# Performance work log

Hardware: AMD Instinct MI355X
Metric: run time of the kernel (lower is better)

Reference implementation:

```python
import jax, jax.numpy as jnp
import numpy as np

N = 10000        # nodes
E = 320000       # edges (avg degree 32)
W = 256          # width (assert width >= 256)
H = 8            # num_head (RESCALE_EDGE assumed (1,1) -> nhead=8, dhead=32)
D = W // H       # per-head dim
BOND = 33        # EMBED_BOND[0]
BAG = 3          # indices per edge bag
EPS_GN = 1e-5


def setup_inputs() -> dict:
    key = jax.random.key(0)
    ks = jax.random.split(key, 12)
    x = jax.random.normal(ks[0], (N, W), dtype=jnp.float32)
    edge_idx = jax.random.randint(ks[1], (2, E), 0, N)
    edge_attr = jax.random.randint(ks[2], (E, BAG), 0, BOND)
    # node in-degree wrt scatter target edge_idx[1], clamped to >= 1
    deg = jax.ops.segment_sum(jnp.ones((E,), jnp.float32), edge_idx[1], num_segments=N)
    deg = jnp.maximum(deg, 1.0)
    s = 1.0 / np.sqrt(W)
    W_src = jax.random.normal(ks[3], (W, W), dtype=jnp.float32) * s
    W_tgt = jax.random.normal(ks[4], (W, W), dtype=jnp.float32) * s
    emb = jax.random.normal(ks[5], (BOND, W), dtype=jnp.float32) * 0.02
    emb = emb.at[0].set(0.0)  # padding_idx=0 row is zeros
    sd = 1.0 / np.sqrt(D)
    W_gate = jax.random.normal(ks[6], (H, D, D), dtype=jnp.float32) * sd  # grouped conv1d k=1
    W_val = jax.random.normal(ks[7], (H, D, D), dtype=jnp.float32) * sd
    W_post = jax.random.normal(ks[8], (W, W), dtype=jnp.float32) * s
    deg_param = jnp.zeros((W,), jnp.float32) - 0.01  # DegreeLayer degree_init
    return {"x": x, "deg": deg, "edge_idx": edge_idx, "edge_attr": edge_attr,
            "W_src": W_src, "W_tgt": W_tgt, "emb": emb,
            "W_gate": W_gate, "W_val": W_val, "W_post": W_post,
            "deg_param": deg_param}


def reference(x, deg, edge_idx, edge_attr, W_src, W_tgt, emb, W_gate, W_val, W_post, deg_param):
    # src/tgt 1x1 Conv1d == per-node linear, then edge gather
    xs = x @ W_src.T                      # [N, W]
    xt = x @ W_tgt.T                      # [N, W]
    xx = xs[edge_idx[0]] + xt[edge_idx[1]]  # [E, W]

    # EmbeddingBag(mode='mean', padding_idx=0): padded entries excluded
    mask = (edge_attr != 0).astype(xx.dtype)            # [E, BAG]
    bag = jnp.einsum('ebc,eb->ec', emb[edge_attr], mask)  # [E, W]
    cnt = jnp.maximum(mask.sum(-1, keepdims=True), 1.0)
    gate_bias = bag / cnt

    # GroupNorm(H, W, affine=False) over [E, W, 1]
    xg = xx.reshape(-1, H, D)
    mu = xg.mean(-1, keepdims=True)
    var = xg.var(-1, keepdims=True)
    xn = (xg - mu) / jnp.sqrt(var + EPS_GN)              # [E, H, D]

    # gated grouped 1x1 convs (dropout is identity at eval)
    gin = xn + gate_bias.reshape(-1, H, D)
    gate = jax.nn.relu(jnp.einsum('ehd,hfd->ehf', gin, W_gate))
    val = jnp.einsum('ehd,hfd->ehf', xn, W_val)
    act = (gate * val).reshape(-1, W)                    # [E, W]
    out_e = act @ W_post.T                               # [E, W]

    # scatter-sum to nodes, then degree rescale
    agg = jax.ops.segment_sum(out_e, edge_idx[1], num_segments=x.shape[0])
    return jnp.power(deg[:, None], deg_param) * agg      # [N, W]
```

## Files before the change

kernel.cpp:

```cpp
#include <hip/hip_runtime.h>

#define WID 256
#define EPS_GN 1e-5f

typedef __bf16 v8bf __attribute__((ext_vector_type(8)));
typedef float  v4f  __attribute__((ext_vector_type(4)));

__device__ inline unsigned short f2b(float f) {
    unsigned int u = __builtin_bit_cast(unsigned int, f);
    unsigned int r = (u + 0x7fffu + ((u >> 16) & 1u)) >> 16;
    return (unsigned short)r;
}
__device__ inline float b2f(unsigned short s) {
    unsigned int u = (unsigned int)s << 16;
    return __builtin_bit_cast(float, u);
}
__device__ inline float lo16(unsigned int u) { return __builtin_bit_cast(float, u << 16); }
__device__ inline float hi16(unsigned int u) { return __builtin_bit_cast(float, u & 0xffff0000u); }

__global__ void prep_k(const float* __restrict__ Wsrc, const float* __restrict__ Wtgt,
                       const float* __restrict__ Wp, const float* __restrict__ Wg,
                       const float* __restrict__ Wv, const float* __restrict__ emb,
                       const int* __restrict__ eidx,
                       unsigned short* __restrict__ Wsb, unsigned short* __restrict__ Wtb,
                       unsigned short* __restrict__ Wpb, unsigned short* __restrict__ Wgb,
                       unsigned short* __restrict__ Wvb, unsigned short* __restrict__ embWgT,
                       int* __restrict__ cnt, int E, int BOND) {
    int b = blockIdx.x, t = threadIdx.x;
    if (b < 256) {
        int i = b * 256 + t;
        Wsb[i] = f2b(Wsrc[i]); Wtb[i] = f2b(Wtgt[i]); Wpb[i] = f2b(Wp[i]);
        if (i < 8192) { Wgb[i] = f2b(Wg[i]); Wvb[i] = f2b(Wv[i]); }
    } else {
        int k = b - 256;
        float s = 0.f;
        if (k < BOND) {
            int h = t >> 5, f = t & 31;
            const float* er = emb + (size_t)k * WID + h * 32;
            const float* wr = Wg + h * 1024 + f * 32;
#pragma unroll
            for (int d = 0; d < 32; d++) s += er[d] * wr[d];
        }
        embWgT[t * 64 + k] = f2b(s);
    }
    for (int i = b * 256 + t; i < E; i += 320 * 256)
        atomicAdd(&cnt[eidx[E + i]], 1);
}

__global__ void scan_k(const int* __restrict__ cnt, int* __restrict__ cur, int N) {
    __shared__ int part[1024];
    int t = threadIdx.x;
    int C = (N + 1023) / 1024;
    int s = 0;
    for (int i = 0; i < C; i++) { int idx = t * C + i; if (idx < N) s += cnt[idx]; }
    part[t] = s;
    __syncthreads();
    for (int d = 1; d < 1024; d <<= 1) {
        int v = (t >= d) ? part[t - d] : 0;
        __syncthreads();
        part[t] += v;
        __syncthreads();
    }
    int base = (t == 0) ? 0 : part[t - 1];
    for (int i = 0; i < C; i++) {
        int idx = t * C + i;
        if (idx < N) { cur[idx] = base; base += cnt[idx]; }
    }
}

__global__ void scat_k(const int* __restrict__ eidx, int* __restrict__ cur,
                       int* __restrict__ perm, int E) {
    int i = blockIdx.x * 256 + threadIdx.x;
    if (i < E) { int p = atomicAdd(&cur[eidx[E + i]], 1); perm[p] = i; }
}

__global__ __launch_bounds__(256, 2)
void proj_k(const float* __restrict__ x, const unsigned short* __restrict__ Wsb,
            const unsigned short* __restrict__ Wtb, unsigned short* __restrict__ xsb,
            unsigned short* __restrict__ xtb, int N) {
    __shared__ unsigned short ab[32 * 264];
    int t = threadIdx.x;
    int n0 = blockIdx.x * 32;
#pragma unroll
    for (int ch = 0; ch < 8; ch++) {
        int flat = ch * 1024 + t * 4;
        int row = flat >> 8, col = flat & 255;
        int n = n0 + row;
        float4 v = (n < N) ? *(const float4*)&x[(size_t)n * WID + col]
                           : make_float4(0.f, 0.f, 0.f, 0.f);
        unsigned int p0 = (unsigned int)f2b(v.x) | ((unsigned int)f2b(v.y) << 16);
        unsigned int p1 = (unsigned int)f2b(v.z) | ((unsigned int)f2b(v.w) << 16);
        *(uint2*)&ab[row * 264 + col] = make_uint2(p0, p1);
    }
    __syncthreads();
    const unsigned short* Wb = blockIdx.y ? Wtb : Wsb;
    unsigned short* outp = blockIdx.y ? xtb : xsb;
    int w = t >> 6, lane = t & 63, m = lane & 15, kg = lane >> 4;
    v4f acc[2][4];
#pragma unroll
    for (int mt = 0; mt < 2; mt++)
#pragma unroll
        for (int nt = 0; nt < 4; nt++) acc[mt][nt] = (v4f){0.f, 0.f, 0.f, 0.f};
#pragma unroll
    for (int kt = 0; kt < 8; kt++) {
        int k0 = kt * 32 + kg * 8;
        v8bf a0 = *(const v8bf*)&ab[m * 264 + k0];
        v8bf a1 = *(const v8bf*)&ab[(16 + m) * 264 + k0];
#pragma unroll
        for (int nt = 0; nt < 4; nt++) {
            int j = w * 64 + nt * 16 + m;
            v8bf b = *(const v8bf*)&Wb[j * 256 + k0];
            acc[0][nt] = __builtin_amdgcn_mfma_f32_16x16x32_bf16(a0, b, acc[0][nt], 0, 0, 0);
            acc[1][nt] = __builtin_amdgcn_mfma_f32_16x16x32_bf16(a1, b, acc[1][nt], 0, 0, 0);
        }
    }
#pragma unroll
    for (int mt = 0; mt < 2; mt++)
#pragma unroll
        for (int r = 0; r < 4; r++) {
            int n = n0 + mt * 16 + kg * 4 + r;
            if (n < N)
#pragma unroll
                for (int nt = 0; nt < 4; nt++)
                    outp[(size_t)n * WID + w * 64 + nt * 16 + m] = f2b(acc[mt][nt][r]);
        }
}

__global__ __launch_bounds__(256, 6)
void edge_k(const unsigned short* __restrict__ xsb, const unsigned short* __restrict__ xtb,
            const int* __restrict__ eidx, const int* __restrict__ eattr,
            const int* __restrict__ perm, const unsigned short* __restrict__ Wgb,
            const unsigned short* __restrict__ Wvb, const unsigned short* __restrict__ embWgT,
            float* __restrict__ aggact, int E) {
    __shared__ unsigned short xxb[32 * 264];
    __shared__ unsigned short Mld[32 * 72];
    __shared__ int src_s[32], tgt_s[32];

    int t = threadIdx.x;
    int e0 = blockIdx.x * 32;
    int ne = min(32, E - e0);

    if (t < 32) {
        int p = (t < ne) ? perm[e0 + t] : -1;
        src_s[t] = (p >= 0) ? eidx[p] : 0;
        tgt_s[t] = (p >= 0) ? eidx[E + p] : 0;
        int a0 = 0, a1 = 0, a2 = 0;
        if (p >= 0) {
            const int* ap = eattr + (size_t)p * 3;
            a0 = ap[0]; a1 = ap[1]; a2 = ap[2];
        }
        unsigned int* Mr = (unsigned int*)&Mld[t * 72];
#pragma unroll
        for (int q = 0; q < 32; q++) Mr[q] = 0;
        int c = (a0 != 0) + (a1 != 0) + (a2 != 0);
        float inv = (p >= 0 && c > 0) ? 1.f / (float)c : 0.f;
        float wa = inv * (float)(1 + (a1 == a0) + (a2 == a0));
        float wb = inv * (float)(1 + (a2 == a1));
        Mld[t * 72 + a0] = f2b(wa);
        if (a1 != a0) Mld[t * 72 + a1] = f2b(wb);
        if (a2 != a0 && a2 != a1) Mld[t * 72 + a2] = f2b(inv);
    }
    __syncthreads();

    {
        int e = t >> 3, c = t & 7;
        int s = src_s[e], g = tgt_s[e];
        bool live = (e < ne);
        const uint4* ps = (const uint4*)(xsb + (size_t)s * WID);
        const uint4* pt = (const uint4*)(xtb + (size_t)g * WID);
        uint4 us[4], ut[4];
#pragma unroll
        for (int i = 0; i < 4; i++) { us[i] = ps[c + 8 * i]; ut[i] = pt[c + 8 * i]; }
        float v[4][8], sum[4], sq[4];
#pragma unroll
        for (int i = 0; i < 4; i++) {
            const unsigned int* au = (const unsigned int*)&us[i];
            const unsigned int* bu = (const unsigned int*)&ut[i];
            sum[i] = 0.f; sq[i] = 0.f;
#pragma unroll
            for (int q = 0; q < 4; q++) {
                float x0 = lo16(au[q]) + lo16(bu[q]);
                float x1 = hi16(au[q]) + hi16(bu[q]);
                if (!live) { x0 = 0.f; x1 = 0.f; }
                v[i][2 * q] = x0; v[i][2 * q + 1] = x1;
                sum[i] += x0 + x1;
                sq[i] += x0 * x0 + x1 * x1;
            }
        }
#pragma unroll
        for (int mask = 1; mask <= 2; mask <<= 1)
#pragma unroll
            for (int i = 0; i < 4; i++) {
                sum[i] += __shfl_xor(sum[i], mask);
                sq[i]  += __shfl_xor(sq[i], mask);
            }
#pragma unroll
        for (int i = 0; i < 4; i++) {
            float mu = sum[i] * (1.f / 32.f);
            float var = sq[i] * (1.f / 32.f) - mu * mu;
            float rs = rsqrtf(var + EPS_GN);
            unsigned int pk[4];
#pragma unroll
            for (int q = 0; q < 4; q++) {
                unsigned int l = f2b((v[i][2 * q] - mu) * rs);
                unsigned int h = f2b((v[i][2 * q + 1] - mu) * rs);
                pk[q] = l | (h << 16);
            }
            *(uint4*)&xxb[e * 264 + (c + 8 * i) * 8] = make_uint4(pk[0], pk[1], pk[2], pk[3]);
        }
    }
    __syncthreads();

    {
        int w = t >> 6, lane = t & 63, m = lane & 15, kg = lane >> 4;
        v8bf axn[2][2], aM[2][2];
#pragma unroll
        for (int mt = 0; mt < 2; mt++) {
            int row = mt * 16 + m;
            axn[0][mt] = *(const v8bf*)&xxb[row * 264 + (w * 2 + 0) * 32 + kg * 8];
            axn[1][mt] = *(const v8bf*)&xxb[row * 264 + (w * 2 + 1) * 32 + kg * 8];
            aM[mt][0] = *(const v8bf*)&Mld[row * 72 + kg * 8];
            aM[mt][1] = *(const v8bf*)&Mld[row * 72 + 32 + kg * 8];
        }
        v4f z = {0.f, 0.f, 0.f, 0.f};
#pragma unroll
        for (int hh = 0; hh < 2; hh++) {
            int h = w * 2 + hh;
#pragma unroll
            for (int nt = 0; nt < 2; nt++) {
                int fj = nt * 16 + m;
                int j = h * 32 + fj;
                v8bf bWg = *(const v8bf*)&Wgb[h * 1024 + fj * 32 + kg * 8];
                v8bf bWv = *(const v8bf*)&Wvb[h * 1024 + fj * 32 + kg * 8];
                v8bf bE0 = *(const v8bf*)&embWgT[j * 64 + kg * 8];
                v8bf bE1 = *(const v8bf*)&embWgT[j * 64 + 32 + kg * 8];
#pragma unroll
                for (int mt = 0; mt < 2; mt++) {
                    v4f cg = __builtin_amdgcn_mfma_f32_16x16x32_bf16(axn[hh][mt], bWg, z, 0, 0, 0);
                    cg = __builtin_amdgcn_mfma_f32_16x16x32_bf16(aM[mt][0], bE0, cg, 0, 0, 0);
                    cg = __builtin_amdgcn_mfma_f32_16x16x32_bf16(aM[mt][1], bE1, cg, 0, 0, 0);
                    v4f cv = __builtin_amdgcn_mfma_f32_16x16x32_bf16(axn[hh][mt], bWv, z, 0, 0, 0);
#pragma unroll
                    for (int r = 0; r < 4; r++) {
                        int e = mt * 16 + kg * 4 + r;
                        xxb[e * 264 + j] = f2b(fmaxf(cg[r], 0.f) * cv[r]);
                    }
                }
            }
        }
    }
    __syncthreads();

    {
        float sum = 0.f;
        int prev = __builtin_amdgcn_readfirstlane(tgt_s[0]);
        for (int e = 0; e < ne; e++) {
            int tg = __builtin_amdgcn_readfirstlane(tgt_s[e]);
            if (tg != prev) {
                atomicAdd(&aggact[(size_t)prev * WID + t], sum);
                sum = 0.f;
                prev = tg;
            }
            sum += b2f(xxb[e * 264 + t]);
        }
        atomicAdd(&aggact[(size_t)prev * WID + t], sum);
    }
}

__global__ __launch_bounds__(256, 2)
void post_k(const float* __restrict__ aggact, const unsigned short* __restrict__ Wpb,
            const float* __restrict__ deg, const float* __restrict__ dp,
            float* __restrict__ out, int N) {
    __shared__ unsigned short ab[32 * 264];
    __shared__ float degl[32];
    int t = threadIdx.x;
    int n0 = blockIdx.x * 32;
#pragma unroll
    for (int ch = 0; ch < 8; ch++) {
        int flat = ch * 1024 + t * 4;
        int row = flat >> 8, col = flat & 255;
        int n = n0 + row;
        float4 v = (n < N) ? *(const float4*)&aggact[(size_t)n * WID + col]
                           : make_float4(0.f, 0.f, 0.f, 0.f);
        unsigned int p0 = (unsigned int)f2b(v.x) | ((unsigned int)f2b(v.y) << 16);
        unsigned int p1 = (unsigned int)f2b(v.z) | ((unsigned int)f2b(v.w) << 16);
        *(uint2*)&ab[row * 264 + col] = make_uint2(p0, p1);
    }
    if (t < 32) {
        int n = n0 + t;
        degl[t] = (n < N) ? log2f(deg[n]) : 0.f;
    }
    __syncthreads();
    int w = t >> 6, lane = t & 63, m = lane & 15, kg = lane >> 4;
    v4f acc[2][4];
#pragma unroll
    for (int mt = 0; mt < 2; mt++)
#pragma unroll
        for (int nt = 0; nt < 4; nt++) acc[mt][nt] = (v4f){0.f, 0.f, 0.f, 0.f};
#pragma unroll
    for (int kt = 0; kt < 8; kt++) {
        int k0 = kt * 32 + kg * 8;
        v8bf a0 = *(const v8bf*)&ab[m * 264 + k0];
        v8bf a1 = *(const v8bf*)&ab[(16 + m) * 264 + k0];
#pragma unroll
        for (int nt = 0; nt < 4; nt++) {
            int j = w * 64 + nt * 16 + m;
            v8bf b = *(const v8bf*)&Wpb[j * 256 + k0];
            acc[0][nt] = __builtin_amdgcn_mfma_f32_16x16x32_bf16(a0, b, acc[0][nt], 0, 0, 0);
            acc[1][nt] = __builtin_amdgcn_mfma_f32_16x16x32_bf16(a1, b, acc[1][nt], 0, 0, 0);
        }
    }
    float dpv[4];
#pragma unroll
    for (int nt = 0; nt < 4; nt++) dpv[nt] = dp[w * 64 + nt * 16 + m];
#pragma unroll
    for (int mt = 0; mt < 2; mt++)
#pragma unroll
        for (int r = 0; r < 4; r++) {
            int row = mt * 16 + kg * 4 + r;
            int n = n0 + row;
            if (n < N) {
                float ld = degl[row];
#pragma unroll
                for (int nt = 0; nt < 4; nt++)
                    out[(size_t)n * WID + w * 64 + nt * 16 + m] =
                        exp2f(dpv[nt] * ld) * acc[mt][nt][r];
            }
        }
}

extern "C" void kernel_launch(void* const* d_in, const int* in_sizes, int n_in,
                              void* d_out, int out_size, void* d_ws, size_t ws_size,
                              hipStream_t stream) {
    const float* x    = (const float*)d_in[0];
    const float* deg  = (const float*)d_in[1];
    const int*   eidx = (const int*)d_in[2];
    const int*   eatt = (const int*)d_in[3];
    const float* Wsrc = (const float*)d_in[4];
    const float* Wtgt = (const float*)d_in[5];
    const float* emb  = (const float*)d_in[6];
    const float* Wg   = (const float*)d_in[7];
    const float* Wv   = (const float*)d_in[8];
    const float* Wp   = (const float*)d_in[9];
    const float* dp   = (const float*)d_in[10];
    int N = in_sizes[0] / WID;
    int E = in_sizes[2] / 2;
    int BOND = in_sizes[6] / WID;

    float* ws     = (float*)d_ws;
    float* aggact = ws;
    int*   cnt    = (int*)(aggact + (size_t)N * WID);
    int*   cur    = cnt + N;
    int*   perm   = cur + N;
    unsigned short* xsb = (unsigned short*)(perm + E);
    unsigned short* xtb = xsb + (size_t)N * WID;
    unsigned short* Wsb = xtb + (size_t)N * WID;
    unsigned short* Wtb = Wsb + 65536;
    unsigned short* Wpb = Wtb + 65536;
    unsigned short* Wgb = Wpb + 65536;
    unsigned short* Wvb = Wgb + 8192;
    unsigned short* embWgT = Wvb + 8192;

    hipMemsetAsync(aggact, 0, ((size_t)N * WID + N) * sizeof(float), stream);
    prep_k<<<320, 256, 0, stream>>>(Wsrc, Wtgt, Wp, Wg, Wv, emb, eidx,
                                    Wsb, Wtb, Wpb, Wgb, Wvb, embWgT, cnt, E, BOND);
    scan_k<<<1, 1024, 0, stream>>>(cnt, cur, N);
    scat_k<<<(E + 255) / 256, 256, 0, stream>>>(eidx, cur, perm, E);
    proj_k<<<dim3((N + 31) / 32, 2), 256, 0, stream>>>(x, Wsb, Wtb, xsb, xtb, N);
    edge_k<<<(E + 31) / 32, 256, 0, stream>>>(xsb, xtb, eidx, eatt, perm, Wgb, Wvb, embWgT, aggact, E);
    post_k<<<(N + 31) / 32, 256, 0, stream>>>(aggact, Wpb, deg, dp, (float*)d_out, N);
}
```

Baseline: 244.0 us.

## Fuse all stages into one cooperative persistent kernel with grid syncs

Replaces the memset plus six separate launches (prep, scan, scatter, proj, edge, post) with one cooperative mega-kernel. Its stages are separated by grid.sync, and the grid is sized from the occupancy query and capped at 1536 blocks. The aim is to remove launch gaps and per-kernel tail effects. The cost is grid-wide barriers, a scan done by a single block while the others wait, and reduced occupancy and parallelism in the edge phase, which now processes contiguous tile chunks per block under a lower launch bound. The old multi-kernel path stays as a fallback if the cooperative launch fails.

```diff
diff --git a/kernel.cpp b/kernel.cpp
--- a/kernel.cpp
+++ b/kernel.cpp
@@ -1,4 +1,7 @@
 #include <hip/hip_runtime.h>
+#include <hip/hip_cooperative_groups.h>
+
+namespace cg = cooperative_groups;
 
 #define WID 256
 #define EPS_GN 1e-5f
@@ -17,6 +20,359 @@
 }
 __device__ inline float lo16(unsigned int u) { return __builtin_bit_cast(float, u << 16); }
 __device__ inline float hi16(unsigned int u) { return __builtin_bit_cast(float, u & 0xffff0000u); }
+
+struct ProjSM { unsigned short ab[32 * 264]; };
+struct EdgeSM {
+    unsigned short xxb[32 * 264];
+    unsigned short Mld[32 * 72];
+    int src_s[32], tgt_s[32];
+};
+struct PostSM { unsigned short ab[32 * 264]; float degl[32]; };
+struct ScanSM { int part[256]; };
+union MegaSM { ProjSM proj; EdgeSM edge; PostSM post; ScanSM scan; };
+
+
+__device__ __forceinline__ void proj_tile(const float* __restrict__ x,
+                                          const unsigned short* __restrict__ Wb,
+                                          unsigned short* __restrict__ outp,
+                                          int N, int n0, int t, ProjSM* s) {
+#pragma unroll
+    for (int ch = 0; ch < 8; ch++) {
+        int flat = ch * 1024 + t * 4;
+        int row = flat >> 8, col = flat & 255;
+        int n = n0 + row;
+        float4 v = (n < N) ? *(const float4*)&x[(size_t)n * WID + col]
+                           : make_float4(0.f, 0.f, 0.f, 0.f);
+        unsigned int p0 = (unsigned int)f2b(v.x) | ((unsigned int)f2b(v.y) << 16);
+        unsigned int p1 = (unsigned int)f2b(v.z) | ((unsigned int)f2b(v.w) << 16);
+        *(uint2*)&s->ab[row * 264 + col] = make_uint2(p0, p1);
+    }
+    __syncthreads();
+    int w = t >> 6, lane = t & 63, m = lane & 15, kg = lane >> 4;
+    v4f acc[2][4];
+#pragma unroll
+    for (int mt = 0; mt < 2; mt++)
+#pragma unroll
+        for (int nt = 0; nt < 4; nt++) acc[mt][nt] = (v4f){0.f, 0.f, 0.f, 0.f};
+#pragma unroll
+    for (int kt = 0; kt < 8; kt++) {
+        int k0 = kt * 32 + kg * 8;
+        v8bf a0 = *(const v8bf*)&s->ab[m * 264 + k0];
+        v8bf a1 = *(const v8bf*)&s->ab[(16 + m) * 264 + k0];
+#pragma unroll
+        for (int nt = 0; nt < 4; nt++) {
+            int j = w * 64 + nt * 16 + m;
+            v8bf b = *(const v8bf*)&Wb[j * 256 + k0];
+            acc[0][nt] = __builtin_amdgcn_mfma_f32_16x16x32_bf16(a0, b, acc[0][nt], 0, 0, 0);
+            acc[1][nt] = __builtin_amdgcn_mfma_f32_16x16x32_bf16(a1, b, acc[1][nt], 0, 0, 0);
+        }
+    }
+#pragma unroll
+    for (int mt = 0; mt < 2; mt++)
+#pragma unroll
+        for (int r = 0; r < 4; r++) {
+            int n = n0 + mt * 16 + kg * 4 + r;
+            if (n < N)
+#pragma unroll
+                for (int nt = 0; nt < 4; nt++)
+                    outp[(size_t)n * WID + w * 64 + nt * 16 + m] = f2b(acc[mt][nt][r]);
+        }
+    __syncthreads();
+}
+
+__device__ __forceinline__ void edge_tile(const unsigned short* __restrict__ xsb,
+                                          const unsigned short* __restrict__ xtb,
+                                          const int* __restrict__ eidx,
+                                          const int* __restrict__ eattr,
+                                          const int* __restrict__ perm,
+                                          const unsigned short* __restrict__ Wgb,
+                                          const unsigned short* __restrict__ Wvb,
+                                          const unsigned short* __restrict__ embWgT,
+                                          float* __restrict__ aggact,
+                                          int E, int e0, int t, EdgeSM* s) {
+    int ne = min(32, E - e0);
+
+    if (t < 32) {
+        int p = (t < ne) ? perm[e0 + t] : -1;
+        s->src_s[t] = (p >= 0) ? eidx[p] : 0;
+        s->tgt_s[t] = (p >= 0) ? eidx[E + p] : 0;
+        int a0 = 0, a1 = 0, a2 = 0;
+        if (p >= 0) {
+            const int* ap = eattr + (size_t)p * 3;
+            a0 = ap[0]; a1 = ap[1]; a2 = ap[2];
+        }
+        unsigned int* Mr = (unsigned int*)&s->Mld[t * 72];
+#pragma unroll
+        for (int q = 0; q < 32; q++) Mr[q] = 0;
+        int c = (a0 != 0) + (a1 != 0) + (a2 != 0);
+        float inv = (p >= 0 && c > 0) ? 1.f / (float)c : 0.f;
+        float wa = inv * (float)(1 + (a1 == a0) + (a2 == a0));
+        float wb = inv * (float)(1 + (a2 == a1));
+        s->Mld[t * 72 + a0] = f2b(wa);
+        if (a1 != a0) s->Mld[t * 72 + a1] = f2b(wb);
+        if (a2 != a0 && a2 != a1) s->Mld[t * 72 + a2] = f2b(inv);
+    }
+    __syncthreads();
+
+    {
+        int e = t >> 3, c = t & 7;
+        int sn = s->src_s[e], g = s->tgt_s[e];
+        bool live = (e < ne);
+        const uint4* ps = (const uint4*)(xsb + (size_t)sn * WID);
+        const uint4* pt = (const uint4*)(xtb + (size_t)g * WID);
+        uint4 us[4], ut[4];
+#pragma unroll
+        for (int i = 0; i < 4; i++) { us[i] = ps[c + 8 * i]; ut[i] = pt[c + 8 * i]; }
+        float v[4][8], sum[4], sq[4];
+#pragma unroll
+        for (int i = 0; i < 4; i++) {
+            const unsigned int* au = (const unsigned int*)&us[i];
+            const unsigned int* bu = (const unsigned int*)&ut[i];
+            sum[i] = 0.f; sq[i] = 0.f;
+#pragma unroll
+            for (int q = 0; q < 4; q++) {
+                float x0 = lo16(au[q]) + lo16(bu[q]);
+                float x1 = hi16(au[q]) + hi16(bu[q]);
+                if (!live) { x0 = 0.f; x1 = 0.f; }
+                v[i][2 * q] = x0; v[i][2 * q + 1] = x1;
+                sum[i] += x0 + x1;
+                sq[i] += x0 * x0 + x1 * x1;
+            }
+        }
+#pragma unroll
+        for (int mask = 1; mask <= 2; mask <<= 1)
+#pragma unroll
+            for (int i = 0; i < 4; i++) {
+                sum[i] += __shfl_xor(sum[i], mask);
+                sq[i]  += __shfl_xor(sq[i], mask);
+            }
+#pragma unroll
+        for (int i = 0; i < 4; i++) {
+            float mu = sum[i] * (1.f / 32.f);
+            float var = sq[i] * (1.f / 32.f) - mu * mu;
+            float rs = rsqrtf(var + EPS_GN);
+            unsigned int pk[4];
+#pragma unroll
+            for (int q = 0; q < 4; q++) {
+                unsigned int l = f2b((v[i][2 * q] - mu) * rs);
+                unsigned int h = f2b((v[i][2 * q + 1] - mu) * rs);
+                pk[q] = l | (h << 16);
+            }
+            *(uint4*)&s->xxb[e * 264 + (c + 8 * i) * 8] = make_uint4(pk[0], pk[1], pk[2], pk[3]);
+        }
+    }
+    __syncthreads();
+
+    {
+        int w = t >> 6, lane = t & 63, m = lane & 15, kg = lane >> 4;
+        v8bf axn[2][2], aM[2][2];
+#pragma unroll
+        for (int mt = 0; mt < 2; mt++) {
+            int row = mt * 16 + m;
+            axn[0][mt] = *(const v8bf*)&s->xxb[row * 264 + (w * 2 + 0) * 32 + kg * 8];
+            axn[1][mt] = *(const v8bf*)&s->xxb[row * 264 + (w * 2 + 1) * 32 + kg * 8];
+            aM[mt][0] = *(const v8bf*)&s->Mld[row * 72 + kg * 8];
+            aM[mt][1] = *(const v8bf*)&s->Mld[row * 72 + 32 + kg * 8];
+        }
+        v4f z = {0.f, 0.f, 0.f, 0.f};
+#pragma unroll
+        for (int hh = 0; hh < 2; hh++) {
+            int h = w * 2 + hh;
+#pragma unroll
+            for (int nt = 0; nt < 2; nt++) {
+                int fj = nt * 16 + m;
+                int j = h * 32 + fj;
+                v8bf bWg = *(const v8bf*)&Wgb[h * 1024 + fj * 32 + kg * 8];
+                v8bf bWv = *(const v8bf*)&Wvb[h * 1024 + fj * 32 + kg * 8];
+                v8bf bE0 = *(const v8bf*)&embWgT[j * 64 + kg * 8];
+                v8bf bE1 = *(const v8bf*)&embWgT[j * 64 + 32 + kg * 8];
+#pragma unroll
+                for (int mt = 0; mt < 2; mt++) {
+                    v4f cgm = __builtin_amdgcn_mfma_f32_16x16x32_bf16(axn[hh][mt], bWg, z, 0, 0, 0);
+                    cgm = __builtin_amdgcn_mfma_f32_16x16x32_bf16(aM[mt][0], bE0, cgm, 0, 0, 0);
+                    cgm = __builtin_amdgcn_mfma_f32_16x16x32_bf16(aM[mt][1], bE1, cgm, 0, 0, 0);
+                    v4f cv = __builtin_amdgcn_mfma_f32_16x16x32_bf16(axn[hh][mt], bWv, z, 0, 0, 0);
+#pragma unroll
+                    for (int r = 0; r < 4; r++) {
+                        int e = mt * 16 + kg * 4 + r;
+                        s->xxb[e * 264 + j] = f2b(fmaxf(cgm[r], 0.f) * cv[r]);
+                    }
+                }
+            }
+        }
+    }
+    __syncthreads();
+
+    {
+        float sum = 0.f;
+        int prev = __builtin_amdgcn_readfirstlane(s->tgt_s[0]);
+        for (int e = 0; e < ne; e++) {
+            int tg = __builtin_amdgcn_readfirstlane(s->tgt_s[e]);
+            if (tg != prev) {
+                atomicAdd(&aggact[(size_t)prev * WID + t], sum);
+                sum = 0.f;
+                prev = tg;
+            }
+            sum += b2f(s->xxb[e * 264 + t]);
+        }
+        atomicAdd(&aggact[(size_t)prev * WID + t], sum);
+    }
+    __syncthreads();
+}
+
+__device__ __forceinline__ void post_tile(const float* __restrict__ aggact,
+                                          const unsigned short* __restrict__ Wpb,
+                                          const float* __restrict__ deg,
+                                          const float* __restrict__ dp,
+                                          float* __restrict__ out,
+                                          int N, int n0, int t, PostSM* s) {
+#pragma unroll
+    for (int ch = 0; ch < 8; ch++) {
+        int flat = ch * 1024 + t * 4;
+        int row = flat >> 8, col = flat & 255;
+        int n = n0 + row;
+        float4 v = (n < N) ? *(const float4*)&aggact[(size_t)n * WID + col]
+                           : make_float4(0.f, 0.f, 0.f, 0.f);
+        unsigned int p0 = (unsigned int)f2b(v.x) | ((unsigned int)f2b(v.y) << 16);
+        unsigned int p1 = (unsigned int)f2b(v.z) | ((unsigned int)f2b(v.w) << 16);
+        *(uint2*)&s->ab[row * 264 + col] = make_uint2(p0, p1);
+    }
+    if (t < 32) {
+        int n = n0 + t;
+        s->degl[t] = (n < N) ? log2f(deg[n]) : 0.f;
+    }
+    __syncthreads();
+    int w = t >> 6, lane = t & 63, m = lane & 15, kg = lane >> 4;
+    v4f acc[2][4];
+#pragma unroll
+    for (int mt = 0; mt < 2; mt++)
+#pragma unroll
+        for (int nt = 0; nt < 4; nt++) acc[mt][nt] = (v4f){0.f, 0.f, 0.f, 0.f};
+#pragma unroll
+    for (int kt = 0; kt < 8; kt++) {
+        int k0 = kt * 32 + kg * 8;
+        v8bf a0 = *(const v8bf*)&s->ab[m * 264 + k0];
+        v8bf a1 = *(const v8bf*)&s->ab[(16 + m) * 264 + k0];
+#pragma unroll
+        for (int nt = 0; nt < 4; nt++) {
+            int j = w * 64 + nt * 16 + m;
+            v8bf b = *(const v8bf*)&Wpb[j * 256 + k0];
+            acc[0][nt] = __builtin_amdgcn_mfma_f32_16x16x32_bf16(a0, b, acc[0][nt], 0, 0, 0);
+            acc[1][nt] = __builtin_amdgcn_mfma_f32_16x16x32_bf16(a1, b, acc[1][nt], 0, 0, 0);
+        }
+    }
+    float dpv[4];
+#pragma unroll
+    for (int nt = 0; nt < 4; nt++) dpv[nt] = dp[w * 64 + nt * 16 + m];
+#pragma unroll
+    for (int mt = 0; mt < 2; mt++)
+#pragma unroll
+        for (int r = 0; r < 4; r++) {
+            int row = mt * 16 + kg * 4 + r;
+            int n = n0 + row;
+            if (n < N) {
+                float ld = s->degl[row];
+#pragma unroll
+                for (int nt = 0; nt < 4; nt++)
+                    out[(size_t)n * WID + w * 64 + nt * 16 + m] =
+                        exp2f(dpv[nt] * ld) * acc[mt][nt][r];
+            }
+        }
+    __syncthreads();
+}
+
+struct MegaArgs {
+    const float *x, *deg, *emb, *Wsrc, *Wtgt, *Wg, *Wv, *Wp, *dp;
+    const int *eidx, *eattr;
+    float *aggact, *out;
+    int *cnt, *cur, *perm;
+    unsigned short *xsb, *xtb, *Wsb, *Wtb, *Wpb, *Wgb, *Wvb, *embWgT;
+    int N, E, BOND;
+};
+
+__global__ __launch_bounds__(256, 4) void mega_k(MegaArgs A) {
+    __shared__ MegaSM sm;
+    cg::grid_group grid = cg::this_grid();
+    int t = threadIdx.x, b = blockIdx.x, G = gridDim.x;
+    int gtid = b * 256 + t, gsz = G * 256;
+
+    for (int i = gtid; i < 65536; i += gsz) {
+        A.Wsb[i] = f2b(A.Wsrc[i]); A.Wtb[i] = f2b(A.Wtgt[i]); A.Wpb[i] = f2b(A.Wp[i]);
+    }
+    for (int i = gtid; i < 8192; i += gsz) { A.Wgb[i] = f2b(A.Wg[i]); A.Wvb[i] = f2b(A.Wv[i]); }
+    for (int i = gtid; i < 16384; i += gsz) {
+        int j = i >> 6, k = i & 63;
+        float sacc = 0.f;
+        if (k < A.BOND) {
+            int h = j >> 5, f = j & 31;
+            const float* er = A.emb + (size_t)k * WID + h * 32;
+            const float* wr = A.Wg + h * 1024 + f * 32;
+#pragma unroll
+            for (int d = 0; d < 32; d++) sacc += er[d] * wr[d];
+        }
+        A.embWgT[j * 64 + k] = f2b(sacc);
+    }
+    {
+        float4* ap = (float4*)A.aggact;
+        int n4 = (A.N * WID) >> 2;
+        for (int i = gtid; i < n4; i += gsz) ap[i] = make_float4(0.f, 0.f, 0.f, 0.f);
+    }
+    for (int i = gtid; i < A.N; i += gsz) A.cnt[i] = 0;
+    grid.sync();
+
+    for (int i = gtid; i < A.E; i += gsz) atomicAdd(&A.cnt[A.eidx[A.E + i]], 1);
+    grid.sync();
+
+    if (b == 0) {
+        int C = (A.N + 255) / 256;
+        int sacc = 0;
+        for (int i = 0; i < C; i++) { int idx = t * C + i; if (idx < A.N) sacc += A.cnt[idx]; }
+        sm.scan.part[t] = sacc;
+        __syncthreads();
+        for (int d = 1; d < 256; d <<= 1) {
+            int v = (t >= d) ? sm.scan.part[t - d] : 0;
+            __syncthreads();
+            sm.scan.part[t] += v;
+            __syncthreads();
+        }
+        int base = (t == 0) ? 0 : sm.scan.part[t - 1];
+        for (int i = 0; i < C; i++) {
+            int idx = t * C + i;
+            if (idx < A.N) { A.cur[idx] = base; base += A.cnt[idx]; }
+        }
+    }
+    grid.sync();
+
+    for (int i = gtid; i < A.E; i += gsz) {
+        int p = atomicAdd(&A.cur[A.eidx[A.E + i]], 1);
+        A.perm[p] = i;
+    }
+    {
+        int ntP = (A.N + 31) / 32;
+        for (int tile = b; tile < 2 * ntP; tile += G) {
+            int pass = (tile >= ntP);
+            int n0 = (tile - pass * ntP) * 32;
+            proj_tile(A.x, pass ? A.Wtb : A.Wsb, pass ? A.xtb : A.xsb, A.N, n0, t, &sm.proj);
+        }
+    }
+    grid.sync();
+
+    {
+        int ntE = (A.E + 31) / 32;
+        int per = (ntE + G - 1) / G;
+        int t0 = b * per, t1 = min(t0 + per, ntE);
+        for (int tile = t0; tile < t1; tile++)
+            edge_tile(A.xsb, A.xtb, A.eidx, A.eattr, A.perm, A.Wgb, A.Wvb, A.embWgT,
+                      A.aggact, A.E, tile * 32, t, &sm.edge);
+    }
+    grid.sync();
+
+    {
+        int ntP = (A.N + 31) / 32;
+        for (int tile = b; tile < ntP; tile += G)
+            post_tile(A.aggact, A.Wpb, A.deg, A.dp, A.out, A.N, tile * 32, t, &sm.post);
+    }
+}
 
 __global__ void prep_k(const float* __restrict__ Wsrc, const float* __restrict__ Wtgt,
                        const float* __restrict__ Wp, const float* __restrict__ Wg,
@@ -78,52 +434,9 @@
 void proj_k(const float* __restrict__ x, const unsigned short* __restrict__ Wsb,
             const unsigned short* __restrict__ Wtb, unsigned short* __restrict__ xsb,
             unsigned short* __restrict__ xtb, int N) {
-    __shared__ unsigned short ab[32 * 264];
-    int t = threadIdx.x;
-    int n0 = blockIdx.x * 32;
-#pragma unroll
-    for (int ch = 0; ch < 8; ch++) {
-        int flat = ch * 1024 + t * 4;
-        int row = flat >> 8, col = flat & 255;
-        int n = n0 + row;
-        float4 v = (n < N) ? *(const float4*)&x[(size_t)n * WID + col]
-                           : make_float4(0.f, 0.f, 0.f, 0.f);
-        unsigned int p0 = (unsigned int)f2b(v.x) | ((unsigned int)f2b(v.y) << 16);
-        unsigned int p1 = (unsigned int)f2b(v.z) | ((unsigned int)f2b(v.w) << 16);
-        *(uint2*)&ab[row * 264 + col] = make_uint2(p0, p1);
-    }
-    __syncthreads();
-    const unsigned short* Wb = blockIdx.y ? Wtb : Wsb;
-    unsigned short* outp = blockIdx.y ? xtb : xsb;
-    int w = t >> 6, lane = t & 63, m = lane & 15, kg = lane >> 4;
-    v4f acc[2][4];
-#pragma unroll
-    for (int mt = 0; mt < 2; mt++)
-#pragma unroll
-        for (int nt = 0; nt < 4; nt++) acc[mt][nt] = (v4f){0.f, 0.f, 0.f, 0.f};
-#pragma unroll
-    for (int kt = 0; kt < 8; kt++) {
-        int k0 = kt * 32 + kg * 8;
-        v8bf a0 = *(const v8bf*)&ab[m * 264 + k0];
-        v8bf a1 = *(const v8bf*)&ab[(16 + m) * 264 + k0];
-#pragma unroll
-        for (int nt = 0; nt < 4; nt++) {
-            int j = w * 64 + nt * 16 + m;
-            v8bf b = *(const v8bf*)&Wb[j * 256 + k0];
-            acc[0][nt] = __builtin_amdgcn_mfma_f32_16x16x32_bf16(a0, b, acc[0][nt], 0, 0, 0);
-            acc[1][nt] = __builtin_amdgcn_mfma_f32_16x16x32_bf16(a1, b, acc[1][nt], 0, 0, 0);
-        }
-    }
-#pragma unroll
-    for (int mt = 0; mt < 2; mt++)
-#pragma unroll
-        for (int r = 0; r < 4; r++) {
-            int n = n0 + mt * 16 + kg * 4 + r;
-            if (n < N)
-#pragma unroll
-                for (int nt = 0; nt < 4; nt++)
-                    outp[(size_t)n * WID + w * 64 + nt * 16 + m] = f2b(acc[mt][nt][r]);
-        }
+    __shared__ ProjSM s;
+    proj_tile(x, blockIdx.y ? Wtb : Wsb, blockIdx.y ? xtb : xsb, N,
+              blockIdx.x * 32, threadIdx.x, &s);
 }
 
 __global__ __launch_bounds__(256, 6)
@@ -132,201 +445,17 @@
             const int* __restrict__ perm, const unsigned short* __restrict__ Wgb,
             const unsigned short* __restrict__ Wvb, const unsigned short* __restrict__ embWgT,
             float* __restrict__ aggact, int E) {
-    __shared__ unsigned short xxb[32 * 264];
-    __shared__ unsigned short Mld[32 * 72];
-    __shared__ int src_s[32], tgt_s[32];
-
-    int t = threadIdx.x;
-    int e0 = blockIdx.x * 32;
-    int ne = min(32, E - e0);
-
-    if (t < 32) {
-        int p = (t < ne) ? perm[e0 + t] : -1;
-        src_s[t] = (p >= 0) ? eidx[p] : 0;
-        tgt_s[t] = (p >= 0) ? eidx[E + p] : 0;
-        int a0 = 0, a1 = 0, a2 = 0;
-        if (p >= 0) {
-            const int* ap = eattr + (size_t)p * 3;
-            a0 = ap[0]; a1 = ap[1]; a2 = ap[2];
-        }
-        unsigned int* Mr = (unsigned int*)&Mld[t * 72];
-#pragma unroll
-        for (int q = 0; q < 32; q++) Mr[q] = 0;
-        int c = (a0 != 0) + (a1 != 0) + (a2 != 0);
-        float inv = (p >= 0 && c > 0) ? 1.f / (float)c : 0.f;
-        float wa = inv * (float)(1 + (a1 == a0) + (a2 == a0));
-        float wb = inv * (float)(1 + (a2 == a1));
-        Mld[t * 72 + a0] = f2b(wa);
-        if (a1 != a0) Mld[t * 72 + a1] = f2b(wb);
-        if (a2 != a0 && a2 != a1) Mld[t * 72 + a2] = f2b(inv);
-    }
-    __syncthreads();
-
-    {
-        int e = t >> 3, c = t & 7;
-        int s = src_s[e], g = tgt_s[e];
-        bool live = (e < ne);
-        const uint4* ps = (const uint4*)(xsb + (size_t)s * WID);
-        const uint4* pt = (const uint4*)(xtb + (size_t)g * WID);
-        uint4 us[4], ut[4];
-#pragma unroll
-        for (int i = 0; i < 4; i++) { us[i] = ps[c + 8 * i]; ut[i] = pt[c + 8 * i]; }
-        float v[4][8], sum[4], sq[4];
-#pragma unroll
-        for (int i = 0; i < 4; i++) {
-            const unsigned int* au = (const unsigned int*)&us[i];
-            const unsigned int* bu = (const unsigned int*)&ut[i];
-            sum[i] = 0.f; sq[i] = 0.f;
-#pragma unroll
-            for (int q = 0; q < 4; q++) {
-                float x0 = lo16(au[q]) + lo16(bu[q]);
-                float x1 = hi16(au[q]) + hi16(bu[q]);
-                if (!live) { x0 = 0.f; x1 = 0.f; }
-                v[i][2 * q] = x0; v[i][2 * q + 1] = x1;
-                sum[i] += x0 + x1;
-                sq[i] += x0 * x0 + x1 * x1;
-            }
-        }
-#pragma unroll
-        for (int mask = 1; mask <= 2; mask <<= 1)
-#pragma unroll
-            for (int i = 0; i < 4; i++) {
-                sum[i] += __shfl_xor(sum[i], mask);
-                sq[i]  += __shfl_xor(sq[i], mask);
-            }
-#pragma unroll
-        for (int i = 0; i < 4; i++) {
-            float mu = sum[i] * (1.f / 32.f);
-            float var = sq[i] * (1.f / 32.f) - mu * mu;
-            float rs = rsqrtf(var + EPS_GN);
-            unsigned int pk[4];
-#pragma unroll
-            for (int q = 0; q < 4; q++) {
-                unsigned int l = f2b((v[i][2 * q] - mu) * rs);
-                unsigned int h = f2b((v[i][2 * q + 1] - mu) * rs);
-                pk[q] = l | (h << 16);
-            }
-            *(uint4*)&xxb[e * 264 + (c + 8 * i) * 8] = make_uint4(pk[0], pk[1], pk[2], pk[3]);
-        }
-    }
-    __syncthreads();
-
-    {
-        int w = t >> 6, lane = t & 63, m = lane & 15, kg = lane >> 4;
-        v8bf axn[2][2], aM[2][2];
-#pragma unroll
-        for (int mt = 0; mt < 2; mt++) {
-            int row = mt * 16 + m;
-            axn[0][mt] = *(const v8bf*)&xxb[row * 264 + (w * 2 + 0) * 32 + kg * 8];
-            axn[1][mt] = *(const v8bf*)&xxb[row * 264 + (w * 2 + 1) * 32 + kg * 8];
-            aM[mt][0] = *(const v8bf*)&Mld[row * 72 + kg * 8];
-            aM[mt][1] = *(const v8bf*)&Mld[row * 72 + 32 + kg * 8];
-        }
-        v4f z = {0.f, 0.f, 0.f, 0.f};
-#pragma unroll
-        for (int hh = 0; hh < 2; hh++) {
-            int h = w * 2 + hh;
-#pragma unroll
-            for (int nt = 0; nt < 2; nt++) {
-                int fj = nt * 16 + m;
-                int j = h * 32 + fj;
-                v8bf bWg = *(const v8bf*)&Wgb[h * 1024 + fj * 32 + kg * 8];
-                v8bf bWv = *(const v8bf*)&Wvb[h * 1024 + fj * 32 + kg * 8];
-                v8bf bE0 = *(const v8bf*)&embWgT[j * 64 + kg * 8];
-                v8bf bE1 = *(const v8bf*)&embWgT[j * 64 + 32 + kg * 8];
-#pragma unroll
-                for (int mt = 0; mt < 2; mt++) {
-                    v4f cg = __builtin_amdgcn_mfma_f32_16x16x32_bf16(axn[hh][mt], bWg, z, 0, 0, 0);
-                    cg = __builtin_amdgcn_mfma_f32_16x16x32_bf16(aM[mt][0], bE0, cg, 0, 0, 0);
-                    cg = __builtin_amdgcn_mfma_f32_16x16x32_bf16(aM[mt][1], bE1, cg, 0, 0, 0);
-                    v4f cv = __builtin_amdgcn_mfma_f32_16x16x32_bf16(axn[hh][mt], bWv, z, 0, 0, 0);
-#pragma unroll
-                    for (int r = 0; r < 4; r++) {
-                        int e = mt * 16 + kg * 4 + r;
-                        xxb[e * 264 + j] = f2b(fmaxf(cg[r], 0.f) * cv[r]);
-                    }
-                }
-            }
-        }
-    }
-    __syncthreads();
-
-    {
-        float sum = 0.f;
-        int prev = __builtin_amdgcn_readfirstlane(tgt_s[0]);
-        for (int e = 0; e < ne; e++) {
-            int tg = __builtin_amdgcn_readfirstlane(tgt_s[e]);
-            if (tg != prev) {
-                atomicAdd(&aggact[(size_t)prev * WID + t], sum);
-                sum = 0.f;
-                prev = tg;
-            }
-            sum += b2f(xxb[e * 264 + t]);
-        }
-        atomicAdd(&aggact[(size_t)prev * WID + t], sum);
-    }
+    __shared__ EdgeSM s;
+    edge_tile(xsb, xtb, eidx, eattr, perm, Wgb, Wvb, embWgT, aggact, E,
+              blockIdx.x * 32, threadIdx.x, &s);
 }
 
 __global__ __launch_bounds__(256, 2)
 void post_k(const float* __restrict__ aggact, const unsigned short* __restrict__ Wpb,
             const float* __restrict__ deg, const float* __restrict__ dp,
             float* __restrict__ out, int N) {
-    __shared__ unsigned short ab[32 * 264];
-    __shared__ float degl[32];
-    int t = threadIdx.x;
-    int n0 = blockIdx.x * 32;
-#pragma unroll
-    for (int ch = 0; ch < 8; ch++) {
-        int flat = ch * 1024 + t * 4;
-        int row = flat >> 8, col = flat & 255;
-        int n = n0 + row;
-        float4 v = (n < N) ? *(const float4*)&aggact[(size_t)n * WID + col]
-                           : make_float4(0.f, 0.f, 0.f, 0.f);
-        unsigned int p0 = (unsigned int)f2b(v.x) | ((unsigned int)f2b(v.y) << 16);
-        unsigned int p1 = (unsigned int)f2b(v.z) | ((unsigned int)f2b(v.w) << 16);
-        *(uint2*)&ab[row * 264 + col] = make_uint2(p0, p1);
-    }
-    if (t < 32) {
-        int n = n0 + t;
-        degl[t] = (n < N) ? log2f(deg[n]) : 0.f;
-    }
-    __syncthreads();
-    int w = t >> 6, lane = t & 63, m = lane & 15, kg = lane >> 4;
-    v4f acc[2][4];
-#pragma unroll
-    for (int mt = 0; mt < 2; mt++)
-#pragma unroll
-        for (int nt = 0; nt < 4; nt++) acc[mt][nt] = (v4f){0.f, 0.f, 0.f, 0.f};
-#pragma unroll
-    for (int kt = 0; kt < 8; kt++) {
-        int k0 = kt * 32 + kg * 8;
-        v8bf a0 = *(const v8bf*)&ab[m * 264 + k0];
-        v8bf a1 = *(const v8bf*)&ab[(16 + m) * 264 + k0];
-#pragma unroll
-        for (int nt = 0; nt < 4; nt++) {
-            int j = w * 64 + nt * 16 + m;
-            v8bf b = *(const v8bf*)&Wpb[j * 256 + k0];
-            acc[0][nt] = __builtin_amdgcn_mfma_f32_16x16x32_bf16(a0, b, acc[0][nt], 0, 0, 0);
-            acc[1][nt] = __builtin_amdgcn_mfma_f32_16x16x32_bf16(a1, b, acc[1][nt], 0, 0, 0);
-        }
-    }
-    float dpv[4];
-#pragma unroll
-    for (int nt = 0; nt < 4; nt++) dpv[nt] = dp[w * 64 + nt * 16 + m];
-#pragma unroll
-    for (int mt = 0; mt < 2; mt++)
-#pragma unroll
-        for (int r = 0; r < 4; r++) {
-            int row = mt * 16 + kg * 4 + r;
-            int n = n0 + row;
-            if (n < N) {
-                float ld = degl[row];
-#pragma unroll
-                for (int nt = 0; nt < 4; nt++)
-                    out[(size_t)n * WID + w * 64 + nt * 16 + m] =
-                        exp2f(dpv[nt] * ld) * acc[mt][nt][r];
-            }
-        }
+    __shared__ PostSM s;
+    post_tile(aggact, Wpb, deg, dp, out, N, blockIdx.x * 32, threadIdx.x, &s);
 }
 
 extern "C" void kernel_launch(void* const* d_in, const int* in_sizes, int n_in,
@@ -361,6 +490,30 @@
     unsigned short* Wvb = Wgb + 8192;
     unsigned short* embWgT = Wvb + 8192;
 
+    bool coop_done = false;
+    {
+        int nb = 0;
+        hipError_t oe = hipOccupancyMaxActiveBlocksPerMultiprocessor(&nb, mega_k, 256, 0);
+        if (oe == hipSuccess && nb > 0) {
+            int G = nb * 256;
+            if (G > 1536) G = 1536;
+            MegaArgs ha;
+            ha.x = x; ha.deg = deg; ha.emb = emb; ha.Wsrc = Wsrc; ha.Wtgt = Wtgt;
+            ha.Wg = Wg; ha.Wv = Wv; ha.Wp = Wp; ha.dp = dp;
+            ha.eidx = eidx; ha.eattr = eatt;
+            ha.aggact = aggact; ha.out = (float*)d_out;
+            ha.cnt = cnt; ha.cur = cur; ha.perm = perm;
+            ha.xsb = xsb; ha.xtb = xtb; ha.Wsb = Wsb; ha.Wtb = Wtb; ha.Wpb = Wpb;
+            ha.Wgb = Wgb; ha.Wvb = Wvb; ha.embWgT = embWgT;
+            ha.N = N; ha.E = E; ha.BOND = BOND;
+            void* kp[] = { &ha };
+            hipError_t le = hipLaunchCooperativeKernel((const void*)mega_k, dim3(G), dim3(256),
+                                                       kp, 0, stream);
+            coop_done = (le == hipSuccess);
+        }
+    }
+    if (coop_done) return;
+
     hipMemsetAsync(aggact, 0, ((size_t)N * WID + N) * sizeof(float), stream);
     prep_k<<<320, 256, 0, stream>>>(Wsrc, Wtgt, Wp, Wg, Wv, emb, eidx,
                                     Wsb, Wtb, Wpb, Wgb, Wvb, embWgT, cnt, E, BOND);
```

Result: slower. 641.9 us (+163.1%).

## Fuse weight prep into projection kernel, move zeroing into scatter, transpose edge LDS

Applied to the files above, without the earlier changes.

The separate weight-conversion kernel and projection kernel are merged into one launch. Projection blocks now convert W_src/W_tgt from fp32 on the fly and compute both projections per block, while extra auxiliary blocks convert the remaining weights and count degrees. Zeroing of the aggregation buffer moves from a memset into the scatter kernel, which cuts launches and memset traffic. In the edge kernel the activation tile in LDS is stored transposed so each thread reads its column contiguously, and the per-edge reduction loop is unrolled. This costs redundant fp32 weight loads and conversions in every projection block, plus an extra barrier.

```diff
diff --git a/kernel.cpp b/kernel.cpp
--- a/kernel.cpp
+++ b/kernel.cpp
@@ -11,6 +11,10 @@
     unsigned int r = (u + 0x7fffu + ((u >> 16) & 1u)) >> 16;
     return (unsigned short)r;
 }
+__device__ inline __bf16 f2bf(float f) {
+    unsigned short s = f2b(f);
+    return __builtin_bit_cast(__bf16, s);
+}
 __device__ inline float b2f(unsigned short s) {
     unsigned int u = (unsigned int)s << 16;
     return __builtin_bit_cast(float, u);
@@ -18,69 +22,47 @@
 __device__ inline float lo16(unsigned int u) { return __builtin_bit_cast(float, u << 16); }
 __device__ inline float hi16(unsigned int u) { return __builtin_bit_cast(float, u & 0xffff0000u); }
 
-__global__ void prep_k(const float* __restrict__ Wsrc, const float* __restrict__ Wtgt,
-                       const float* __restrict__ Wp, const float* __restrict__ Wg,
-                       const float* __restrict__ Wv, const float* __restrict__ emb,
-                       const int* __restrict__ eidx,
-                       unsigned short* __restrict__ Wsb, unsigned short* __restrict__ Wtb,
-                       unsigned short* __restrict__ Wpb, unsigned short* __restrict__ Wgb,
-                       unsigned short* __restrict__ Wvb, unsigned short* __restrict__ embWgT,
-                       int* __restrict__ cnt, int E, int BOND) {
-    int b = blockIdx.x, t = threadIdx.x;
-    if (b < 256) {
-        int i = b * 256 + t;
-        Wsb[i] = f2b(Wsrc[i]); Wtb[i] = f2b(Wtgt[i]); Wpb[i] = f2b(Wp[i]);
-        if (i < 8192) { Wgb[i] = f2b(Wg[i]); Wvb[i] = f2b(Wv[i]); }
-    } else {
-        int k = b - 256;
-        float s = 0.f;
-        if (k < BOND) {
-            int h = t >> 5, f = t & 31;
-            const float* er = emb + (size_t)k * WID + h * 32;
-            const float* wr = Wg + h * 1024 + f * 32;
-#pragma unroll
-            for (int d = 0; d < 32; d++) s += er[d] * wr[d];
-        }
-        embWgT[t * 64 + k] = f2b(s);
-    }
-    for (int i = b * 256 + t; i < E; i += 320 * 256)
-        atomicAdd(&cnt[eidx[E + i]], 1);
-}
-
-__global__ void scan_k(const int* __restrict__ cnt, int* __restrict__ cur, int N) {
-    __shared__ int part[1024];
-    int t = threadIdx.x;
-    int C = (N + 1023) / 1024;
-    int s = 0;
-    for (int i = 0; i < C; i++) { int idx = t * C + i; if (idx < N) s += cnt[idx]; }
-    part[t] = s;
-    __syncthreads();
-    for (int d = 1; d < 1024; d <<= 1) {
-        int v = (t >= d) ? part[t - d] : 0;
-        __syncthreads();
-        part[t] += v;
-        __syncthreads();
-    }
-    int base = (t == 0) ? 0 : part[t - 1];
-    for (int i = 0; i < C; i++) {
-        int idx = t * C + i;
-        if (idx < N) { cur[idx] = base; base += cnt[idx]; }
-    }
-}
-
-__global__ void scat_k(const int* __restrict__ eidx, int* __restrict__ cur,
-                       int* __restrict__ perm, int E) {
-    int i = blockIdx.x * 256 + threadIdx.x;
-    if (i < E) { int p = atomicAdd(&cur[eidx[E + i]], 1); perm[p] = i; }
+__device__ inline v8bf ld_w8(const float* __restrict__ p) {
+    float4 a = *(const float4*)p, b = *(const float4*)(p + 4);
+    v8bf r;
+    r[0] = f2bf(a.x); r[1] = f2bf(a.y); r[2] = f2bf(a.z); r[3] = f2bf(a.w);
+    r[4] = f2bf(b.x); r[5] = f2bf(b.y); r[6] = f2bf(b.z); r[7] = f2bf(b.w);
+    return r;
 }
 
 __global__ __launch_bounds__(256, 2)
-void proj_k(const float* __restrict__ x, const unsigned short* __restrict__ Wsb,
-            const unsigned short* __restrict__ Wtb, unsigned short* __restrict__ xsb,
-            unsigned short* __restrict__ xtb, int N) {
+void prepproj_k(const float* __restrict__ x, const float* __restrict__ Wsrc,
+                const float* __restrict__ Wtgt, const float* __restrict__ Wp,
+                const float* __restrict__ Wg, const float* __restrict__ Wv,
+                const float* __restrict__ emb, const int* __restrict__ eidx,
+                unsigned short* __restrict__ xsb, unsigned short* __restrict__ xtb,
+                unsigned short* __restrict__ Wpb, unsigned short* __restrict__ Wgb,
+                unsigned short* __restrict__ Wvb, unsigned short* __restrict__ embWgT,
+                int* __restrict__ cnt, int N, int E, int BOND, int PB, int AUX) {
     __shared__ unsigned short ab[32 * 264];
-    int t = threadIdx.x;
-    int n0 = blockIdx.x * 32;
+    int t = threadIdx.x, b = blockIdx.x;
+
+    if (b >= PB) {
+        int atid = (b - PB) * 256 + t, asz = AUX * 256;
+        for (int i = atid; i < 65536; i += asz) Wpb[i] = f2b(Wp[i]);
+        for (int i = atid; i < 8192; i += asz) { Wgb[i] = f2b(Wg[i]); Wvb[i] = f2b(Wv[i]); }
+        for (int i = atid; i < 16384; i += asz) {
+            int j = i >> 6, k = i & 63;
+            float sacc = 0.f;
+            if (k < BOND) {
+                int h = j >> 5, f = j & 31;
+                const float* er = emb + (size_t)k * WID + h * 32;
+                const float* wr = Wg + h * 1024 + f * 32;
+#pragma unroll
+                for (int d = 0; d < 32; d++) sacc += er[d] * wr[d];
+            }
+            embWgT[j * 64 + k] = f2b(sacc);
+        }
+        for (int i = atid; i < E; i += asz) atomicAdd(&cnt[eidx[E + i]], 1);
+        return;
+    }
+
+    int n0 = b * 32;
 #pragma unroll
     for (int ch = 0; ch < 8; ch++) {
         int flat = ch * 1024 + t * 4;
@@ -93,37 +75,72 @@
         *(uint2*)&ab[row * 264 + col] = make_uint2(p0, p1);
     }
     __syncthreads();
-    const unsigned short* Wb = blockIdx.y ? Wtb : Wsb;
-    unsigned short* outp = blockIdx.y ? xtb : xsb;
     int w = t >> 6, lane = t & 63, m = lane & 15, kg = lane >> 4;
-    v4f acc[2][4];
-#pragma unroll
-    for (int mt = 0; mt < 2; mt++)
-#pragma unroll
-        for (int nt = 0; nt < 4; nt++) acc[mt][nt] = (v4f){0.f, 0.f, 0.f, 0.f};
-#pragma unroll
-    for (int kt = 0; kt < 8; kt++) {
-        int k0 = kt * 32 + kg * 8;
-        v8bf a0 = *(const v8bf*)&ab[m * 264 + k0];
-        v8bf a1 = *(const v8bf*)&ab[(16 + m) * 264 + k0];
-#pragma unroll
-        for (int nt = 0; nt < 4; nt++) {
-            int j = w * 64 + nt * 16 + m;
-            v8bf b = *(const v8bf*)&Wb[j * 256 + k0];
-            acc[0][nt] = __builtin_amdgcn_mfma_f32_16x16x32_bf16(a0, b, acc[0][nt], 0, 0, 0);
-            acc[1][nt] = __builtin_amdgcn_mfma_f32_16x16x32_bf16(a1, b, acc[1][nt], 0, 0, 0);
-        }
-    }
-#pragma unroll
-    for (int mt = 0; mt < 2; mt++)
-#pragma unroll
-        for (int r = 0; r < 4; r++) {
-            int n = n0 + mt * 16 + kg * 4 + r;
-            if (n < N)
-#pragma unroll
-                for (int nt = 0; nt < 4; nt++)
-                    outp[(size_t)n * WID + w * 64 + nt * 16 + m] = f2b(acc[mt][nt][r]);
-        }
+#pragma unroll
+    for (int pass = 0; pass < 2; pass++) {
+        const float* Wf = pass ? Wtgt : Wsrc;
+        unsigned short* outp = pass ? xtb : xsb;
+        v4f acc[2][4];
+#pragma unroll
+        for (int mt = 0; mt < 2; mt++)
+#pragma unroll
+            for (int nt = 0; nt < 4; nt++) acc[mt][nt] = (v4f){0.f, 0.f, 0.f, 0.f};
+#pragma unroll
+        for (int kt = 0; kt < 8; kt++) {
+            int k0 = kt * 32 + kg * 8;
+            v8bf a0 = *(const v8bf*)&ab[m * 264 + k0];
+            v8bf a1 = *(const v8bf*)&ab[(16 + m) * 264 + k0];
+#pragma unroll
+            for (int nt = 0; nt < 4; nt++) {
+                int j = w * 64 + nt * 16 + m;
+                v8bf bfr = ld_w8(&Wf[j * 256 + k0]);
+                acc[0][nt] = __builtin_amdgcn_mfma_f32_16x16x32_bf16(a0, bfr, acc[0][nt], 0, 0, 0);
+                acc[1][nt] = __builtin_amdgcn_mfma_f32_16x16x32_bf16(a1, bfr, acc[1][nt], 0, 0, 0);
+            }
+        }
+#pragma unroll
+        for (int mt = 0; mt < 2; mt++)
+#pragma unroll
+            for (int r = 0; r < 4; r++) {
+                int n = n0 + mt * 16 + kg * 4 + r;
+                if (n < N)
+#pragma unroll
+                    for (int nt = 0; nt < 4; nt++)
+                        outp[(size_t)n * WID + w * 64 + nt * 16 + m] = f2b(acc[mt][nt][r]);
+            }
+    }
+}
+
+__global__ void scan_k(const int* __restrict__ cnt, int* __restrict__ cur, int N) {
+    __shared__ int part[1024];
+    int t = threadIdx.x;
+    int C = (N + 1023) / 1024;
+    int s = 0;
+    for (int i = 0; i < C; i++) { int idx = t * C + i; if (idx < N) s += cnt[idx]; }
+    part[t] = s;
+    __syncthreads();
+    for (int d = 1; d < 1024; d <<= 1) {
+        int v = (t >= d) ? part[t - d] : 0;
+        __syncthreads();
+        part[t] += v;
+        __syncthreads();
+    }
+    int base = (t == 0) ? 0 : part[t - 1];
+    for (int i = 0; i < C; i++) {
+        int idx = t * C + i;
+        if (idx < N) { cur[idx] = base; base += cnt[idx]; }
+    }
+}
+
+__global__ void scat_k(const int* __restrict__ eidx, int* __restrict__ cur,
+                       int* __restrict__ perm, float* __restrict__ aggact,
+                       int E, int N) {
+    int i = blockIdx.x * 256 + threadIdx.x;
+    int gsz = gridDim.x * 256;
+    float4* ap = (float4*)aggact;
+    int n4 = (N * WID) >> 2;
+    for (int j = i; j < n4; j += gsz) ap[j] = make_float4(0.f, 0.f, 0.f, 0.f);
+    if (i < E) { int p = atomicAdd(&cur[eidx[E + i]], 1); perm[p] = i; }
 }
 
 __global__ __launch_bounds__(256, 6)
@@ -132,7 +149,7 @@
             const int* __restrict__ perm, const unsigned short* __restrict__ Wgb,
             const unsigned short* __restrict__ Wvb, const unsigned short* __restrict__ embWgT,
             float* __restrict__ aggact, int E) {
-    __shared__ unsigned short xxb[32 * 264];
+    __shared__ unsigned short xxb[9216];
     __shared__ unsigned short Mld[32 * 72];
     __shared__ int src_s[32], tgt_s[32];
 
@@ -164,9 +181,9 @@
 
     {
         int e = t >> 3, c = t & 7;
-        int s = src_s[e], g = tgt_s[e];
+        int sn = src_s[e], g = tgt_s[e];
         bool live = (e < ne);
-        const uint4* ps = (const uint4*)(xsb + (size_t)s * WID);
+        const uint4* ps = (const uint4*)(xsb + (size_t)sn * WID);
         const uint4* pt = (const uint4*)(xtb + (size_t)g * WID);
         uint4 us[4], ut[4];
 #pragma unroll
@@ -222,6 +239,7 @@
             aM[mt][0] = *(const v8bf*)&Mld[row * 72 + kg * 8];
             aM[mt][1] = *(const v8bf*)&Mld[row * 72 + 32 + kg * 8];
         }
+        __syncthreads();
         v4f z = {0.f, 0.f, 0.f, 0.f};
 #pragma unroll
         for (int hh = 0; hh < 2; hh++) {
@@ -236,14 +254,14 @@
                 v8bf bE1 = *(const v8bf*)&embWgT[j * 64 + 32 + kg * 8];
 #pragma unroll
                 for (int mt = 0; mt < 2; mt++) {
-                    v4f cg = __builtin_amdgcn_mfma_f32_16x16x32_bf16(axn[hh][mt], bWg, z, 0, 0, 0);
-                    cg = __builtin_amdgcn_mfma_f32_16x16x32_bf16(aM[mt][0], bE0, cg, 0, 0, 0);
-                    cg = __builtin_amdgcn_mfma_f32_16x16x32_bf16(aM[mt][1], bE1, cg, 0, 0, 0);
+                    v4f cgm = __builtin_amdgcn_mfma_f32_16x16x32_bf16(axn[hh][mt], bWg, z, 0, 0, 0);
+                    cgm = __builtin_amdgcn_mfma_f32_16x16x32_bf16(aM[mt][0], bE0, cgm, 0, 0, 0);
+                    cgm = __builtin_amdgcn_mfma_f32_16x16x32_bf16(aM[mt][1], bE1, cgm, 0, 0, 0);
                     v4f cv = __builtin_amdgcn_mfma_f32_16x16x32_bf16(axn[hh][mt], bWv, z, 0, 0, 0);
 #pragma unroll
                     for (int r = 0; r < 4; r++) {
                         int e = mt * 16 + kg * 4 + r;
-                        xxb[e * 264 + j] = f2b(fmaxf(cg[r], 0.f) * cv[r]);
+                        xxb[j * 36 + e] = f2b(fmaxf(cgm[r], 0.f) * cv[r]);
                     }
                 }
             }
@@ -252,16 +270,27 @@
     __syncthreads();
 
     {
+        uint2 raw[8];
+#pragma unroll
+        for (int i = 0; i < 8; i++) raw[i] = *(const uint2*)&xxb[t * 36 + i * 4];
+        float col[32];
+#pragma unroll
+        for (int i = 0; i < 8; i++) {
+            col[4 * i + 0] = lo16(raw[i].x); col[4 * i + 1] = hi16(raw[i].x);
+            col[4 * i + 2] = lo16(raw[i].y); col[4 * i + 3] = hi16(raw[i].y);
+        }
         float sum = 0.f;
         int prev = __builtin_amdgcn_readfirstlane(tgt_s[0]);
-        for (int e = 0; e < ne; e++) {
+#pragma unroll
+        for (int e = 0; e < 32; e++) {
+            if (e >= ne) break;
             int tg = __builtin_amdgcn_readfirstlane(tgt_s[e]);
             if (tg != prev) {
                 atomicAdd(&aggact[(size_t)prev * WID + t], sum);
                 sum = 0.f;
                 prev = tg;
             }
-            sum += b2f(xxb[e * 264 + t]);
+            sum += col[e];
         }
         atomicAdd(&aggact[(size_t)prev * WID + t], sum);
     }
@@ -354,19 +383,20 @@
     int*   perm   = cur + N;
     unsigned short* xsb = (unsigned short*)(perm + E);
     unsigned short* xtb = xsb + (size_t)N * WID;
-    unsigned short* Wsb = xtb + (size_t)N * WID;
-    unsigned short* Wtb = Wsb + 65536;
-    unsigned short* Wpb = Wtb + 65536;
+    unsigned short* Wpb = xtb + (size_t)N * WID;
     unsigned short* Wgb = Wpb + 65536;
     unsigned short* Wvb = Wgb + 8192;
     unsigned short* embWgT = Wvb + 8192;
 
-    hipMemsetAsync(aggact, 0, ((size_t)N * WID + N) * sizeof(float), stream);
-    prep_k<<<320, 256, 0, stream>>>(Wsrc, Wtgt, Wp, Wg, Wv, emb, eidx,
-                                    Wsb, Wtb, Wpb, Wgb, Wvb, embWgT, cnt, E, BOND);
+    int PB = (N + 31) / 32;
+    int AUX = 128;
+
+    hipMemsetAsync(cnt, 0, (size_t)N * sizeof(int), stream);
+    prepproj_k<<<PB + AUX, 256, 0, stream>>>(x, Wsrc, Wtgt, Wp, Wg, Wv, emb, eidx,
+                                             xsb, xtb, Wpb, Wgb, Wvb, embWgT, cnt,
+                                             N, E, BOND, PB, AUX);
     scan_k<<<1, 1024, 0, stream>>>(cnt, cur, N);
-    scat_k<<<(E + 255) / 256, 256, 0, stream>>>(eidx, cur, perm, E);
-    proj_k<<<dim3((N + 31) / 32, 2), 256, 0, stream>>>(x, Wsb, Wtb, xsb, xtb, N);
+    scat_k<<<(E + 255) / 256, 256, 0, stream>>>(eidx, cur, perm, aggact, E, N);
     edge_k<<<(E + 31) / 32, 256, 0, stream>>>(xsb, xtb, eidx, eatt, perm, Wgb, Wvb, embWgT, aggact, E);
     post_k<<<(N + 31) / 32, 256, 0, stream>>>(aggact, Wpb, deg, dp, (float*)d_out, N);
 }
```

Result: slower. 350.1 us (+43.5%).
